# Kernel optimization log

Hardware: AMD Instinct MI355X
Metric: run time of the kernel (lower is better)

## Reference

```python
import jax, jax.numpy as jnp
import numpy as np

D_MODEL = 768
N_HEAD = 12
D_FF = 3072
EPS = 1e-5


def _layer_norm(x, w, b):
    mu = jnp.mean(x, axis=-1, keepdims=True)
    var = jnp.mean(jnp.square(x - mu), axis=-1, keepdims=True)
    return (x - mu) * jax.lax.rsqrt(var + EPS) * w + b


def setup_inputs() -> dict:
    key = jax.random.key(0)
    ks = jax.random.split(key, 8)
    B, S, D = 2, 4096, D_MODEL
    s_in = 1.0 / np.sqrt(D)
    s_ff = 1.0 / np.sqrt(D_FF)
    return {
        "src": jax.random.normal(ks[0], (B, S, D), jnp.float32),
        "w_qkv": jax.random.uniform(ks[1], (3 * D, D), jnp.float32, -s_in, s_in),
        "b_qkv": jnp.zeros((3 * D,), jnp.float32),
        "w_out": jax.random.uniform(ks[2], (D, D), jnp.float32, -s_in, s_in),
        "b_out": jnp.zeros((D,), jnp.float32),
        "w1": jax.random.uniform(ks[3], (D_FF, D), jnp.float32, -s_in, s_in),
        "b1": jnp.zeros((D_FF,), jnp.float32),
        "w2": jax.random.uniform(ks[4], (D, D_FF), jnp.float32, -s_ff, s_ff),
        "b2": jnp.zeros((D,), jnp.float32),
        "ln1_w": jnp.ones((D,), jnp.float32),
        "ln1_b": jnp.zeros((D,), jnp.float32),
        "ln2_w": jnp.ones((D,), jnp.float32),
        "ln2_b": jnp.zeros((D,), jnp.float32),
    }


def reference(src, w_qkv, b_qkv, w_out, b_out, w1, b1, w2, b2,
              ln1_w, ln1_b, ln2_w, ln2_b):
    B, S, D = src.shape
    H, dh = N_HEAD, D // N_HEAD
    # fused QKV projection: [B,S,3D]
    qkv = jnp.einsum('bsd,ed->bse', src, w_qkv) + b_qkv
    q, k, v = jnp.split(qkv, 3, axis=-1)
    q = q.reshape(B, S, H, dh)
    k = k.reshape(B, S, H, dh)
    v = v.reshape(B, S, H, dh)
    scale = 1.0 / np.sqrt(dh)
    scores = jnp.einsum('bqhd,bkhd->bhqk', q, k) * scale  # [B,H,S,S]
    attn = jax.nn.softmax(scores, axis=-1)
    ctx = jnp.einsum('bhqk,bkhd->bqhd', attn, v).reshape(B, S, D)
    attn_out = jnp.einsum('bsd,ed->bse', ctx, w_out) + b_out
    # post-norm residual (norm_first=False), dropout inactive in eval
    x = _layer_norm(src + attn_out, ln1_w, ln1_b)
    h = jax.nn.relu(jnp.einsum('bsd,fd->bsf', x, w1) + b1)
    ffn = jnp.einsum('bsf,df->bsd', h, w2) + b2
    return _layer_norm(x + ffn, ln2_w, ln2_b)
```

## Files before the change

kernel.cpp:

```cpp
#include <hip/hip_runtime.h>
#include <hip/hip_bf16.h>

typedef __hip_bfloat16 bf16;
typedef __attribute__((ext_vector_type(8))) short s16x8;
typedef __attribute__((ext_vector_type(4))) float f32x4;

#define MFMA16x16x32(A, B, C) __builtin_amdgcn_mfma_f32_16x16x32_bf16((A), (B), (C), 0, 0, 0)

__device__ __forceinline__ void async_copy16(const bf16* g, bf16* l) {
  __builtin_amdgcn_global_load_lds(
      (const __attribute__((address_space(1))) void*)g,
      (__attribute__((address_space(3))) void*)l, 16, 0, 0);
}

__device__ __forceinline__ float swz_x16(float x) {
  return __int_as_float(__builtin_amdgcn_ds_swizzle(__float_as_int(x), 0x401f));
}

__device__ __forceinline__ int SW(int row, int chunk) {
  return row * 64 + (((chunk) ^ (row & 7)) << 3);
}

__global__ __launch_bounds__(256)
void cast_f2b_kernel(const float* __restrict__ in, bf16* __restrict__ out, int n) {
  const int i = (blockIdx.x * 256 + threadIdx.x) * 4;
  if (i < n) {
    const float4 f = *(const float4*)(in + i);
    out[i + 0] = (bf16)f.x; out[i + 1] = (bf16)f.y;
    out[i + 2] = (bf16)f.z; out[i + 3] = (bf16)f.w;
  }
}

template <int RELU, int VT, int ACCUM, typename OutT>
__global__ __launch_bounds__(256)
void gemm_bt_kernel(const bf16* __restrict__ A, const bf16* __restrict__ B,
                    const float* __restrict__ bias, OutT* __restrict__ C,
                    int N, int K, int ldb) {
  __shared__ __align__(16) bf16 As[128 * 32];
  __shared__ __align__(16) bf16 Bs[128 * 32];

  const int t = threadIdx.x;
  const int lane = t & 63;
  const int wave = t >> 6;
  const int wm = (wave >> 1) << 6;
  const int wn = (wave & 1) << 6;
  const int col16 = lane & 15;
  const int quad = lane >> 4;
  const int bm = blockIdx.x;
  const int bn = blockIdx.y;

  const bf16* Ag = A + (size_t)(bm * 128 + (t >> 2)) * K + (t & 3) * 8;
  const bf16* Bg = B + (size_t)(bn * 128 + (t >> 2)) * ldb + (t & 3) * 8;
  bf16* Asd = As + t * 8;
  bf16* Bsd = Bs + t * 8;

  f32x4 acc[4][4] = {};

  for (int k0 = 0; k0 < K; k0 += 32) {
    __syncthreads();
    async_copy16(Ag + k0, Asd);
    async_copy16(Ag + (size_t)64 * K + k0, Asd + 2048);
    async_copy16(Bg + k0, Bsd);
    async_copy16(Bg + (size_t)64 * ldb + k0, Bsd + 2048);
    asm volatile("s_waitcnt vmcnt(0)" ::: "memory");
    __syncthreads();

    s16x8 af[4], bfr[4];
#pragma unroll
    for (int i = 0; i < 4; i++)
      af[i] = *(const s16x8*)(As + (wm + i * 16 + col16) * 32 + quad * 8);
#pragma unroll
    for (int j = 0; j < 4; j++)
      bfr[j] = *(const s16x8*)(Bs + (wn + j * 16 + col16) * 32 + quad * 8);
#pragma unroll
    for (int i = 0; i < 4; i++)
#pragma unroll
      for (int j = 0; j < 4; j++)
        acc[i][j] = MFMA16x16x32(af[i], bfr[j], acc[i][j]);
  }

  const int row0 = bm * 128 + wm + quad * 4;
  const int col0 = bn * 128 + wn + col16;
#pragma unroll
  for (int j = 0; j < 4; j++) {
    const int col = col0 + j * 16;
    const float bv = ACCUM ? 0.0f : bias[col];
#pragma unroll
    for (int i = 0; i < 4; i++) {
#pragma unroll
      for (int r = 0; r < 4; r++) {
        float v = acc[i][j][r] + bv;
        if (RELU) v = fmaxf(v, 0.0f);
        const int row = row0 + i * 16 + r;
        if (VT) {
          ((bf16*)C)[(size_t)((row >> 12) * 12 + (col >> 6)) * 262144 +
                     (col & 63) * 4096 + (row & 4095)] = (bf16)v;
        } else {
          const size_t idx = (size_t)row * N + col;
          if (ACCUM) v += ((const float*)C)[idx];
          C[idx] = (OutT)v;
        }
      }
    }
  }
}

__global__ __launch_bounds__(256)
void attn_kernel(const bf16* __restrict__ QK, const bf16* __restrict__ Vt,
                 bf16* __restrict__ ctx) {
  __shared__ __align__(16) bf16 Ks[64 * 64];
  __shared__ __align__(16) bf16 Vs[64 * 64];
  __shared__ __align__(16) bf16 Ps[4][32 * 64];

  const int t = threadIdx.x, lane = t & 63, wave = t >> 6;
  const int col16 = lane & 15, quad = lane >> 4;
  const int b = blockIdx.z, h = blockIdx.y;
  const int qw0 = blockIdx.x * 128 + wave * 32;

  s16x8 bq[2][2];
#pragma unroll
  for (int qt = 0; qt < 2; qt++)
#pragma unroll
    for (int s = 0; s < 2; s++) {
      union { s16x8 v; bf16 hh[8]; } u;
      u.v = *(const s16x8*)(QK + (size_t)(b * 4096 + qw0 + qt * 16 + col16) * 1536 +
                            h * 64 + s * 32 + quad * 8);
#pragma unroll
      for (int e = 0; e < 8; e++) u.hh[e] = (bf16)((float)u.hh[e] * 0.18033688f);
      bq[qt][s] = u.v;
    }

  const bf16* kbase = QK + (size_t)(b * 4096) * 1536 + 768 + h * 64;
  const bf16* vbase = Vt + (size_t)(b * 12 + h) * 262144;
  const int srow = t >> 2;
  const int cch = t & 3;

  f32x4 o[4][2] = {};
  float l_[2] = {0.0f, 0.0f};
  bf16* pw = &Ps[wave][0];

  for (int k0 = 0; k0 < 4096; k0 += 64) {
    const s16x8 kc0 = *(const s16x8*)(kbase + (size_t)(k0 + srow) * 1536 + cch * 8);
    const s16x8 kc1 = *(const s16x8*)(kbase + (size_t)(k0 + srow) * 1536 + cch * 8 + 32);
    const s16x8 vc0 = *(const s16x8*)(vbase + (size_t)srow * 4096 + k0 + cch * 8);
    const s16x8 vc1 = *(const s16x8*)(vbase + (size_t)srow * 4096 + k0 + cch * 8 + 32);
    __syncthreads();
    *(s16x8*)(Ks + SW(srow, cch)) = kc0;
    *(s16x8*)(Ks + SW(srow, cch + 4)) = kc1;
    *(s16x8*)(Vs + SW(srow, cch)) = vc0;
    *(s16x8*)(Vs + SW(srow, cch + 4)) = vc1;
    __syncthreads();

    f32x4 st[4][2] = {};
#pragma unroll
    for (int s = 0; s < 2; s++) {
      s16x8 ak[4];
#pragma unroll
      for (int kt = 0; kt < 4; kt++)
        ak[kt] = *(const s16x8*)(Ks + SW(kt * 16 + col16, s * 4 + quad));
#pragma unroll
      for (int kt = 0; kt < 4; kt++)
#pragma unroll
        for (int qt = 0; qt < 2; qt++)
          st[kt][qt] = MFMA16x16x32(ak[kt], bq[qt][s], st[kt][qt]);
    }

#pragma unroll
    for (int qt = 0; qt < 2; qt++) {
#pragma unroll
      for (int kt = 0; kt < 4; kt++) {
        union { unsigned long long u; bf16 hh[4]; } pk;
#pragma unroll
        for (int r = 0; r < 4; r++) {
          const float p = exp2f(st[kt][qt][r] - 16.0f);
          l_[qt] += p;
          pk.hh[r] = (bf16)p;
        }
        *(unsigned long long*)(pw + (qt * 16 + col16) * 64 +
                               (((kt * 2 + (quad >> 1)) ^ (col16 & 7)) << 3) +
                               (quad & 1) * 4) = pk.u;
      }
    }
    asm volatile("s_waitcnt lgkmcnt(0)" ::: "memory");

#pragma unroll
    for (int s = 0; s < 2; s++) {
      s16x8 bp[2];
#pragma unroll
      for (int qt = 0; qt < 2; qt++)
        bp[qt] = *(const s16x8*)(pw + SW(qt * 16 + col16, s * 4 + quad));
#pragma unroll
      for (int dt = 0; dt < 4; dt++) {
        const s16x8 av = *(const s16x8*)(Vs + SW(dt * 16 + col16, s * 4 + quad));
#pragma unroll
        for (int qt = 0; qt < 2; qt++)
          o[dt][qt] = MFMA16x16x32(av, bp[qt], o[dt][qt]);
      }
    }
  }

  float inv[2];
#pragma unroll
  for (int qt = 0; qt < 2; qt++) {
    float l = l_[qt];
    l += swz_x16(l);
    l += __shfl_xor(l, 32, 64);
    inv[qt] = 1.0f / l;
  }

#pragma unroll
  for (int qt = 0; qt < 2; qt++)
#pragma unroll
    for (int dt = 0; dt < 4; dt++)
#pragma unroll
      for (int r = 0; r < 4; r++)
        pw[(qt * 16 + col16) * 64 + (((dt * 2 + (quad >> 1)) ^ (col16 & 7)) << 3) +
           (quad & 1) * 4 + r] = (bf16)(o[dt][qt][r] * inv[qt]);
  asm volatile("s_waitcnt lgkmcnt(0)" ::: "memory");
  const int qrow = lane >> 1, chalf = (lane & 1) * 4;
  bf16* dst = ctx + (size_t)(b * 4096 + qw0 + qrow) * 768 + h * 64 + chalf * 8;
#pragma unroll
  for (int i = 0; i < 4; i++)
    *(s16x8*)(dst + i * 8) = *(const s16x8*)(pw + SW(qrow, chalf + i));
}

__global__ __launch_bounds__(256)
void add_ln_b_kernel(const float* __restrict__ X, const float* __restrict__ Y,
                     const float* __restrict__ w, const float* __restrict__ b,
                     bf16* __restrict__ out) {
  const int row = blockIdx.x * 4 + (threadIdx.x >> 6);
  const int lane = threadIdx.x & 63;
  const float* x = X + (size_t)row * 768;
  const float* y = Y + (size_t)row * 768;
  float v[12];
  float s = 0.0f;
#pragma unroll
  for (int i = 0; i < 3; i++) {
    const int c = lane * 4 + i * 256;
    const float4 xf = *(const float4*)(x + c);
    const float4 yf = *(const float4*)(y + c);
    v[i * 4 + 0] = xf.x + yf.x; v[i * 4 + 1] = xf.y + yf.y;
    v[i * 4 + 2] = xf.z + yf.z; v[i * 4 + 3] = xf.w + yf.w;
    s += v[i * 4] + v[i * 4 + 1] + v[i * 4 + 2] + v[i * 4 + 3];
  }
#pragma unroll
  for (int off = 32; off > 0; off >>= 1) s += __shfl_xor(s, off, 64);
  const float mu = s * (1.0f / 768.0f);
  float var = 0.0f;
#pragma unroll
  for (int i = 0; i < 12; i++) { const float d = v[i] - mu; var += d * d; }
#pragma unroll
  for (int off = 32; off > 0; off >>= 1) var += __shfl_xor(var, off, 64);
  const float rs = rsqrtf(var * (1.0f / 768.0f) + 1e-5f);
#pragma unroll
  for (int i = 0; i < 12; i++) {
    const int c = lane * 4 + (i >> 2) * 256 + (i & 3);
    out[(size_t)row * 768 + c] = (bf16)((v[i] - mu) * rs * w[c] + b[c]);
  }
}

__global__ __launch_bounds__(256)
void add_ln_f_kernel(const bf16* __restrict__ X, const float* __restrict__ Y,
                     const float* __restrict__ w, const float* __restrict__ b,
                     float* __restrict__ out) {
  const int row = blockIdx.x * 4 + (threadIdx.x >> 6);
  const int lane = threadIdx.x & 63;
  const bf16* x = X + (size_t)row * 768;
  const float* y = Y + (size_t)row * 768;
  float v[12];
  float s = 0.0f;
#pragma unroll
  for (int i = 0; i < 3; i++) {
    const int c = lane * 4 + i * 256;
    const float4 yf = *(const float4*)(y + c);
    v[i * 4 + 0] = (float)x[c + 0] + yf.x; v[i * 4 + 1] = (float)x[c + 1] + yf.y;
    v[i * 4 + 2] = (float)x[c + 2] + yf.z; v[i * 4 + 3] = (float)x[c + 3] + yf.w;
    s += v[i * 4] + v[i * 4 + 1] + v[i * 4 + 2] + v[i * 4 + 3];
  }
#pragma unroll
  for (int off = 32; off > 0; off >>= 1) s += __shfl_xor(s, off, 64);
  const float mu = s * (1.0f / 768.0f);
  float var = 0.0f;
#pragma unroll
  for (int i = 0; i < 12; i++) { const float d = v[i] - mu; var += d * d; }
#pragma unroll
  for (int off = 32; off > 0; off >>= 1) var += __shfl_xor(var, off, 64);
  const float rs = rsqrtf(var * (1.0f / 768.0f) + 1e-5f);
#pragma unroll
  for (int i = 0; i < 12; i++) {
    const int c = lane * 4 + (i >> 2) * 256 + (i & 3);
    out[(size_t)row * 768 + c] = (v[i] - mu) * rs * w[c] + b[c];
  }
}

extern "C" void kernel_launch(void* const* d_in, const int* in_sizes, int n_in,
                              void* d_out, int out_size, void* d_ws, size_t ws_size,
                              hipStream_t stream) {
  (void)in_sizes; (void)n_in; (void)out_size; (void)ws_size;
  const float* src   = (const float*)d_in[0];
  const float* w_qkv = (const float*)d_in[1];
  const float* b_qkv = (const float*)d_in[2];
  const float* w_out = (const float*)d_in[3];
  const float* b_out = (const float*)d_in[4];
  const float* w1    = (const float*)d_in[5];
  const float* b1    = (const float*)d_in[6];
  const float* w2    = (const float*)d_in[7];
  const float* b2    = (const float*)d_in[8];
  const float* ln1w  = (const float*)d_in[9];
  const float* ln1b  = (const float*)d_in[10];
  const float* ln2w  = (const float*)d_in[11];
  const float* ln2b  = (const float*)d_in[12];
  float* out = (float*)d_out;

  char* ws = (char*)d_ws;
  bf16* wqkvb = (bf16*)ws;
  bf16* woutb = (bf16*)(ws + 3538944);
  bf16* w1b   = (bf16*)(ws + 4718592);
  bf16* w2b   = (bf16*)(ws + 9437184);
  bf16* srcb  = (bf16*)(ws + 14155776);
  bf16* QK    = (bf16*)(ws + 26738688);
  bf16* Vt    = (bf16*)(ws + 51904512);
  bf16* ctx   = (bf16*)d_out;
  float* attn_out = (float*)(ws + 26738688);
  bf16* x1b   = (bf16*)(ws + 51904512);
  bf16* hbuf  = (bf16*)(ws + 14155776);
  float* ffn  = out;

  cast_f2b_kernel<<<1728, 256, 0, stream>>>(w_qkv, wqkvb, 2304 * 768);
  cast_f2b_kernel<<<576,  256, 0, stream>>>(w_out, woutb, 768 * 768);
  cast_f2b_kernel<<<2304, 256, 0, stream>>>(w1, w1b, 3072 * 768);
  cast_f2b_kernel<<<2304, 256, 0, stream>>>(w2, w2b, 768 * 3072);
  cast_f2b_kernel<<<6144, 256, 0, stream>>>(src, srcb, 8192 * 768);

  gemm_bt_kernel<0, 0, 0, bf16><<<dim3(64, 12), 256, 0, stream>>>(
      srcb, wqkvb, b_qkv, QK, 1536, 768, 768);
  gemm_bt_kernel<0, 1, 0, bf16><<<dim3(64, 6), 256, 0, stream>>>(
      srcb, wqkvb + (size_t)1536 * 768, b_qkv + 1536, Vt, 768, 768, 768);
  attn_kernel<<<dim3(32, 12, 2), 256, 0, stream>>>(QK, Vt, ctx);
  gemm_bt_kernel<0, 0, 0, float><<<dim3(64, 6), 256, 0, stream>>>(
      ctx, woutb, b_out, attn_out, 768, 768, 768);
  add_ln_b_kernel<<<2048, 256, 0, stream>>>(src, attn_out, ln1w, ln1b, x1b);
  for (int c = 0; c < 2; c++) {
    gemm_bt_kernel<1, 0, 0, bf16><<<dim3(64, 12), 256, 0, stream>>>(
        x1b, w1b + (size_t)c * 1536 * 768, b1 + c * 1536, hbuf, 1536, 768, 768);
    if (c == 0)
      gemm_bt_kernel<0, 0, 0, float><<<dim3(64, 6), 256, 0, stream>>>(
          hbuf, w2b + c * 1536, b2, ffn, 768, 1536, 3072);
    else
      gemm_bt_kernel<0, 0, 1, float><<<dim3(64, 6), 256, 0, stream>>>(
          hbuf, w2b + c * 1536, b2, ffn, 768, 1536, 3072);
  }
  add_ln_f_kernel<<<2048, 256, 0, stream>>>(x1b, ffn, ln2w, ln2b, out);
}
```

Measured before the change: 536.1 us.

## Split attention keys across wave pairs, fuse QKV GEMMs and weight casts

The attention kernel now gives each wave 64 queries and half of each 64-key tile, so K and V fragments loaded from LDS are reused across four query tiles instead of two. The two key-half partial outputs and row sums are merged through LDS at the end, with the partial output rounded to bf16 before the merge. The Q/K and V projection GEMMs are fused into one launch that routes output columns to row-major QK or transposed V, and the five cast launches are merged into one. This cuts LDS traffic and launch count, at the cost of more registers per wave, a slower epilogue where half the waves idle, and some extra rounding error.

```diff
diff --git a/kernel.cpp b/kernel.cpp
--- a/kernel.cpp
+++ b/kernel.cpp
@@ -20,34 +20,40 @@
 __device__ __forceinline__ int SW(int row, int chunk) {
   return row * 64 + (((chunk) ^ (row & 7)) << 3);
 }
-
-__global__ __launch_bounds__(256)
-void cast_f2b_kernel(const float* __restrict__ in, bf16* __restrict__ out, int n) {
-  const int i = (blockIdx.x * 256 + threadIdx.x) * 4;
-  if (i < n) {
-    const float4 f = *(const float4*)(in + i);
-    out[i + 0] = (bf16)f.x; out[i + 1] = (bf16)f.y;
-    out[i + 2] = (bf16)f.z; out[i + 3] = (bf16)f.w;
-  }
-}
-
-template <int RELU, int VT, int ACCUM, typename OutT>
+__device__ __forceinline__ int SW32(int row, int chunk) {
+  return row * 32 + (((chunk) ^ (row & 3)) << 3);
+}
+
+__global__ __launch_bounds__(256)
+void cast_all_kernel(const float* __restrict__ p0, bf16* __restrict__ q0,
+                     const float* __restrict__ p1, bf16* __restrict__ q1,
+                     const float* __restrict__ p2, bf16* __restrict__ q2,
+                     const float* __restrict__ p3, bf16* __restrict__ q3,
+                     const float* __restrict__ p4, bf16* __restrict__ q4) {
+  int blk = blockIdx.x;
+  const float* in; bf16* out;
+  if (blk < 1728)      { in = p0; out = q0; }
+  else if (blk < 2304) { in = p1; out = q1; blk -= 1728; }
+  else if (blk < 4608) { in = p2; out = q2; blk -= 2304; }
+  else if (blk < 6912) { in = p3; out = q3; blk -= 4608; }
+  else                 { in = p4; out = q4; blk -= 6912; }
+  const int i = (blk * 256 + threadIdx.x) * 4;
+  const float4 f = *(const float4*)(in + i);
+  out[i + 0] = (bf16)f.x; out[i + 1] = (bf16)f.y;
+  out[i + 2] = (bf16)f.z; out[i + 3] = (bf16)f.w;
+}
+
+template <int RELU, int ACCUM, typename OutT>
 __global__ __launch_bounds__(256)
 void gemm_bt_kernel(const bf16* __restrict__ A, const bf16* __restrict__ B,
                     const float* __restrict__ bias, OutT* __restrict__ C,
                     int N, int K, int ldb) {
   __shared__ __align__(16) bf16 As[128 * 32];
   __shared__ __align__(16) bf16 Bs[128 * 32];
-
-  const int t = threadIdx.x;
-  const int lane = t & 63;
-  const int wave = t >> 6;
-  const int wm = (wave >> 1) << 6;
-  const int wn = (wave & 1) << 6;
-  const int col16 = lane & 15;
-  const int quad = lane >> 4;
-  const int bm = blockIdx.x;
-  const int bn = blockIdx.y;
+  const int t = threadIdx.x, lane = t & 63, wave = t >> 6;
+  const int wm = (wave >> 1) << 6, wn = (wave & 1) << 6;
+  const int col16 = lane & 15, quad = lane >> 4;
+  const int bm = blockIdx.x, bn = blockIdx.y;
 
   const bf16* Ag = A + (size_t)(bm * 128 + (t >> 2)) * K + (t & 3) * 8;
   const bf16* Bg = B + (size_t)(bn * 128 + (t >> 2)) * ldb + (t & 3) * 8;
@@ -55,7 +61,6 @@
   bf16* Bsd = Bs + t * 8;
 
   f32x4 acc[4][4] = {};
-
   for (int k0 = 0; k0 < K; k0 += 32) {
     __syncthreads();
     async_copy16(Ag + k0, Asd);
@@ -64,7 +69,6 @@
     async_copy16(Bg + (size_t)64 * ldb + k0, Bsd + 2048);
     asm volatile("s_waitcnt vmcnt(0)" ::: "memory");
     __syncthreads();
-
     s16x8 af[4], bfr[4];
 #pragma unroll
     for (int i = 0; i < 4; i++)
@@ -78,7 +82,6 @@
       for (int j = 0; j < 4; j++)
         acc[i][j] = MFMA16x16x32(af[i], bfr[j], acc[i][j]);
   }
-
   const int row0 = bm * 128 + wm + quad * 4;
   const int col0 = bn * 128 + wn + col16;
 #pragma unroll
@@ -86,44 +89,101 @@
     const int col = col0 + j * 16;
     const float bv = ACCUM ? 0.0f : bias[col];
 #pragma unroll
-    for (int i = 0; i < 4; i++) {
+    for (int i = 0; i < 4; i++)
 #pragma unroll
       for (int r = 0; r < 4; r++) {
         float v = acc[i][j][r] + bv;
         if (RELU) v = fmaxf(v, 0.0f);
+        const size_t idx = (size_t)(row0 + i * 16 + r) * N + col;
+        if (ACCUM) v += ((const float*)C)[idx];
+        C[idx] = (OutT)v;
+      }
+  }
+}
+
+__global__ __launch_bounds__(256)
+void gemm_qkv_kernel(const bf16* __restrict__ A, const bf16* __restrict__ B,
+                     const float* __restrict__ bias, bf16* __restrict__ QKo,
+                     bf16* __restrict__ Vt) {
+  __shared__ __align__(16) bf16 As[128 * 32];
+  __shared__ __align__(16) bf16 Bs[128 * 32];
+  const int t = threadIdx.x, lane = t & 63, wave = t >> 6;
+  const int wm = (wave >> 1) << 6, wn = (wave & 1) << 6;
+  const int col16 = lane & 15, quad = lane >> 4;
+  const int bm = blockIdx.x, bn = blockIdx.y;
+  const int K = 768;
+
+  const bf16* Ag = A + (size_t)(bm * 128 + (t >> 2)) * K + (t & 3) * 8;
+  const bf16* Bg = B + (size_t)(bn * 128 + (t >> 2)) * K + (t & 3) * 8;
+  bf16* Asd = As + t * 8;
+  bf16* Bsd = Bs + t * 8;
+
+  f32x4 acc[4][4] = {};
+  for (int k0 = 0; k0 < K; k0 += 32) {
+    __syncthreads();
+    async_copy16(Ag + k0, Asd);
+    async_copy16(Ag + (size_t)64 * K + k0, Asd + 2048);
+    async_copy16(Bg + k0, Bsd);
+    async_copy16(Bg + (size_t)64 * K + k0, Bsd + 2048);
+    asm volatile("s_waitcnt vmcnt(0)" ::: "memory");
+    __syncthreads();
+    s16x8 af[4], bfr[4];
+#pragma unroll
+    for (int i = 0; i < 4; i++)
+      af[i] = *(const s16x8*)(As + (wm + i * 16 + col16) * 32 + quad * 8);
+#pragma unroll
+    for (int j = 0; j < 4; j++)
+      bfr[j] = *(const s16x8*)(Bs + (wn + j * 16 + col16) * 32 + quad * 8);
+#pragma unroll
+    for (int i = 0; i < 4; i++)
+#pragma unroll
+      for (int j = 0; j < 4; j++)
+        acc[i][j] = MFMA16x16x32(af[i], bfr[j], acc[i][j]);
+  }
+  const int row0 = bm * 128 + wm + quad * 4;
+  const int col0 = bn * 128 + wn + col16;
+#pragma unroll
+  for (int j = 0; j < 4; j++) {
+    const int col = col0 + j * 16;
+    const float bv = bias[col];
+#pragma unroll
+    for (int i = 0; i < 4; i++)
+#pragma unroll
+      for (int r = 0; r < 4; r++) {
+        const float v = acc[i][j][r] + bv;
         const int row = row0 + i * 16 + r;
-        if (VT) {
-          ((bf16*)C)[(size_t)((row >> 12) * 12 + (col >> 6)) * 262144 +
-                     (col & 63) * 4096 + (row & 4095)] = (bf16)v;
+        if (bn < 12) {
+          QKo[(size_t)row * 1536 + col] = (bf16)v;
         } else {
-          const size_t idx = (size_t)row * N + col;
-          if (ACCUM) v += ((const float*)C)[idx];
-          C[idx] = (OutT)v;
+          const int vc = col - 1536;
+          Vt[(size_t)((row >> 12) * 12 + (vc >> 6)) * 262144 +
+             (vc & 63) * 4096 + (row & 4095)] = (bf16)v;
         }
       }
-    }
   }
 }
 
 __global__ __launch_bounds__(256)
 void attn_kernel(const bf16* __restrict__ QK, const bf16* __restrict__ Vt,
                  bf16* __restrict__ ctx) {
-  __shared__ __align__(16) bf16 Ks[64 * 64];
-  __shared__ __align__(16) bf16 Vs[64 * 64];
-  __shared__ __align__(16) bf16 Ps[4][32 * 64];
+  __shared__ __align__(16) bf16 lds[16384];
+  bf16* Ks = lds;
+  bf16* Vs = lds + 4096;
+  bf16* Ps = lds + 8192;
 
   const int t = threadIdx.x, lane = t & 63, wave = t >> 6;
   const int col16 = lane & 15, quad = lane >> 4;
+  const int qh = wave >> 1, kh = wave & 1;
   const int b = blockIdx.z, h = blockIdx.y;
-  const int qw0 = blockIdx.x * 128 + wave * 32;
-
-  s16x8 bq[2][2];
-#pragma unroll
-  for (int qt = 0; qt < 2; qt++)
+  const int qbase = blockIdx.x * 128 + qh * 64;
+
+  s16x8 bq[4][2];
+#pragma unroll
+  for (int qt = 0; qt < 4; qt++)
 #pragma unroll
     for (int s = 0; s < 2; s++) {
       union { s16x8 v; bf16 hh[8]; } u;
-      u.v = *(const s16x8*)(QK + (size_t)(b * 4096 + qw0 + qt * 16 + col16) * 1536 +
+      u.v = *(const s16x8*)(QK + (size_t)(b * 4096 + qbase + qt * 16 + col16) * 1536 +
                             h * 64 + s * 32 + quad * 8);
 #pragma unroll
       for (int e = 0; e < 8; e++) u.hh[e] = (bf16)((float)u.hh[e] * 0.18033688f);
@@ -132,12 +192,11 @@
 
   const bf16* kbase = QK + (size_t)(b * 4096) * 1536 + 768 + h * 64;
   const bf16* vbase = Vt + (size_t)(b * 12 + h) * 262144;
-  const int srow = t >> 2;
-  const int cch = t & 3;
-
-  f32x4 o[4][2] = {};
-  float l_[2] = {0.0f, 0.0f};
-  bf16* pw = &Ps[wave][0];
+  const int srow = t >> 2, cch = t & 3;
+
+  f32x4 o[4][4] = {};
+  float l_[4] = {};
+  bf16* pw = Ps + wave * 2048;
 
   for (int k0 = 0; k0 < 4096; k0 += 64) {
     const s16x8 kc0 = *(const s16x8*)(kbase + (size_t)(k0 + srow) * 1536 + cch * 8);
@@ -151,24 +210,25 @@
     *(s16x8*)(Vs + SW(srow, cch + 4)) = vc1;
     __syncthreads();
 
-    f32x4 st[4][2] = {};
+    f32x4 st[2][4] = {};
 #pragma unroll
     for (int s = 0; s < 2; s++) {
-      s16x8 ak[4];
-#pragma unroll
-      for (int kt = 0; kt < 4; kt++)
-        ak[kt] = *(const s16x8*)(Ks + SW(kt * 16 + col16, s * 4 + quad));
-#pragma unroll
-      for (int kt = 0; kt < 4; kt++)
-#pragma unroll
-        for (int qt = 0; qt < 2; qt++)
+      s16x8 ak[2];
+#pragma unroll
+      for (int kt = 0; kt < 2; kt++)
+        ak[kt] = *(const s16x8*)(Ks + SW(kh * 32 + kt * 16 + col16, s * 4 + quad));
+#pragma unroll
+      for (int kt = 0; kt < 2; kt++)
+#pragma unroll
+        for (int qt = 0; qt < 4; qt++)
           st[kt][qt] = MFMA16x16x32(ak[kt], bq[qt][s], st[kt][qt]);
     }
 
 #pragma unroll
-    for (int qt = 0; qt < 2; qt++) {
-#pragma unroll
-      for (int kt = 0; kt < 4; kt++) {
+    for (int qt = 0; qt < 4; qt++) {
+      const int q32 = qt * 16 + col16;
+#pragma unroll
+      for (int kt = 0; kt < 2; kt++) {
         union { unsigned long long u; bf16 hh[4]; } pk;
 #pragma unroll
         for (int r = 0; r < 4; r++) {
@@ -176,52 +236,84 @@
           l_[qt] += p;
           pk.hh[r] = (bf16)p;
         }
-        *(unsigned long long*)(pw + (qt * 16 + col16) * 64 +
-                               (((kt * 2 + (quad >> 1)) ^ (col16 & 7)) << 3) +
+        const int chunk = kt * 2 + (quad >> 1);
+        *(unsigned long long*)(pw + q32 * 32 + ((chunk ^ (q32 & 3)) << 3) +
                                (quad & 1) * 4) = pk.u;
       }
     }
     asm volatile("s_waitcnt lgkmcnt(0)" ::: "memory");
 
-#pragma unroll
-    for (int s = 0; s < 2; s++) {
-      s16x8 bp[2];
-#pragma unroll
-      for (int qt = 0; qt < 2; qt++)
-        bp[qt] = *(const s16x8*)(pw + SW(qt * 16 + col16, s * 4 + quad));
+    s16x8 bp[4];
+#pragma unroll
+    for (int qt = 0; qt < 4; qt++)
+      bp[qt] = *(const s16x8*)(pw + SW32(qt * 16 + col16, quad));
+#pragma unroll
+    for (int dt = 0; dt < 4; dt++) {
+      const s16x8 av = *(const s16x8*)(Vs + SW(dt * 16 + col16, kh * 4 + quad));
+#pragma unroll
+      for (int qt = 0; qt < 4; qt++)
+        o[dt][qt] = MFMA16x16x32(av, bp[qt], o[dt][qt]);
+    }
+  }
+
+  __syncthreads();
+  bf16* mb = lds;
+  float* lb = (float*)(lds + 8192);
+  if (kh == 1) {
+#pragma unroll
+    for (int qt = 0; qt < 4; qt++) {
+      const int q = qt * 16 + col16;
+#pragma unroll
+      for (int dt = 0; dt < 4; dt++)
+#pragma unroll
+        for (int r = 0; r < 4; r++)
+          mb[qh * 4096 + q * 64 + dt * 16 + quad * 4 + r] = (bf16)o[dt][qt][r];
+      lb[qh * 1024 + q * 4 + quad] = l_[qt];
+    }
+  }
+  __syncthreads();
+  if (kh == 0) {
+    float inv[4];
+#pragma unroll
+    for (int qt = 0; qt < 4; qt++) {
+      const int q = qt * 16 + col16;
+      float l = l_[qt] + lb[qh * 1024 + q * 4 + quad];
+      l += swz_x16(l);
+      l += __shfl_xor(l, 32, 64);
+      inv[qt] = 1.0f / l;
+    }
+#pragma unroll
+    for (int qt = 0; qt < 4; qt++) {
+      const int q = qt * 16 + col16;
+#pragma unroll
+      for (int dt = 0; dt < 4; dt++)
+#pragma unroll
+        for (int r = 0; r < 4; r++)
+          o[dt][qt][r] += (float)mb[qh * 4096 + q * 64 + dt * 16 + quad * 4 + r];
+    }
+    asm volatile("s_waitcnt lgkmcnt(0)" ::: "memory");
+    bf16* tr = lds + 8192 + qh * 4096;
+#pragma unroll
+    for (int qt = 0; qt < 4; qt++) {
+      const int q = qt * 16 + col16;
 #pragma unroll
       for (int dt = 0; dt < 4; dt++) {
-        const s16x8 av = *(const s16x8*)(Vs + SW(dt * 16 + col16, s * 4 + quad));
-#pragma unroll
-        for (int qt = 0; qt < 2; qt++)
-          o[dt][qt] = MFMA16x16x32(av, bp[qt], o[dt][qt]);
+        union { unsigned long long u; bf16 hh[4]; } pk;
+#pragma unroll
+        for (int r = 0; r < 4; r++) pk.hh[r] = (bf16)(o[dt][qt][r] * inv[qt]);
+        const int chunk = dt * 2 + (quad >> 1);
+        *(unsigned long long*)(tr + q * 64 + ((chunk ^ (q & 7)) << 3) +
+                               (quad & 1) * 4) = pk.u;
       }
     }
-  }
-
-  float inv[2];
-#pragma unroll
-  for (int qt = 0; qt < 2; qt++) {
-    float l = l_[qt];
-    l += swz_x16(l);
-    l += __shfl_xor(l, 32, 64);
-    inv[qt] = 1.0f / l;
-  }
-
-#pragma unroll
-  for (int qt = 0; qt < 2; qt++)
-#pragma unroll
-    for (int dt = 0; dt < 4; dt++)
-#pragma unroll
-      for (int r = 0; r < 4; r++)
-        pw[(qt * 16 + col16) * 64 + (((dt * 2 + (quad >> 1)) ^ (col16 & 7)) << 3) +
-           (quad & 1) * 4 + r] = (bf16)(o[dt][qt][r] * inv[qt]);
-  asm volatile("s_waitcnt lgkmcnt(0)" ::: "memory");
-  const int qrow = lane >> 1, chalf = (lane & 1) * 4;
-  bf16* dst = ctx + (size_t)(b * 4096 + qw0 + qrow) * 768 + h * 64 + chalf * 8;
-#pragma unroll
-  for (int i = 0; i < 4; i++)
-    *(s16x8*)(dst + i * 8) = *(const s16x8*)(pw + SW(qrow, chalf + i));
+    asm volatile("s_waitcnt lgkmcnt(0)" ::: "memory");
+    bf16* dst = ctx + (size_t)(b * 4096 + qbase + lane) * 768 + h * 64;
+#pragma unroll
+    for (int p = 0; p < 8; p++) {
+      const s16x8 val = *(const s16x8*)(tr + lane * 64 + (p << 3));
+      *(s16x8*)(dst + (p ^ (lane & 7)) * 8) = val;
+    }
+  }
 }
 
 __global__ __launch_bounds__(256)
@@ -232,16 +324,14 @@
   const int lane = threadIdx.x & 63;
   const float* x = X + (size_t)row * 768;
   const float* y = Y + (size_t)row * 768;
-  float v[12];
-  float s = 0.0f;
+  float v[12]; float s = 0.0f;
 #pragma unroll
   for (int i = 0; i < 3; i++) {
     const int c = lane * 4 + i * 256;
     const float4 xf = *(const float4*)(x + c);
     const float4 yf = *(const float4*)(y + c);
-    v[i * 4 + 0] = xf.x + yf.x; v[i * 4 + 1] = xf.y + yf.y;
-    v[i * 4 + 2] = xf.z + yf.z; v[i * 4 + 3] = xf.w + yf.w;
-    s += v[i * 4] + v[i * 4 + 1] + v[i * 4 + 2] + v[i * 4 + 3];
+    v[i*4+0]=xf.x+yf.x; v[i*4+1]=xf.y+yf.y; v[i*4+2]=xf.z+yf.z; v[i*4+3]=xf.w+yf.w;
+    s += v[i*4]+v[i*4+1]+v[i*4+2]+v[i*4+3];
   }
 #pragma unroll
   for (int off = 32; off > 0; off >>= 1) s += __shfl_xor(s, off, 64);
@@ -267,15 +357,14 @@
   const int lane = threadIdx.x & 63;
   const bf16* x = X + (size_t)row * 768;
   const float* y = Y + (size_t)row * 768;
-  float v[12];
-  float s = 0.0f;
+  float v[12]; float s = 0.0f;
 #pragma unroll
   for (int i = 0; i < 3; i++) {
     const int c = lane * 4 + i * 256;
     const float4 yf = *(const float4*)(y + c);
-    v[i * 4 + 0] = (float)x[c + 0] + yf.x; v[i * 4 + 1] = (float)x[c + 1] + yf.y;
-    v[i * 4 + 2] = (float)x[c + 2] + yf.z; v[i * 4 + 3] = (float)x[c + 3] + yf.w;
-    s += v[i * 4] + v[i * 4 + 1] + v[i * 4 + 2] + v[i * 4 + 3];
+    v[i*4+0]=(float)x[c+0]+yf.x; v[i*4+1]=(float)x[c+1]+yf.y;
+    v[i*4+2]=(float)x[c+2]+yf.z; v[i*4+3]=(float)x[c+3]+yf.w;
+    s += v[i*4]+v[i*4+1]+v[i*4+2]+v[i*4+3];
   }
 #pragma unroll
   for (int off = 32; off > 0; off >>= 1) s += __shfl_xor(s, off, 64);
@@ -326,28 +415,21 @@
   bf16* hbuf  = (bf16*)(ws + 14155776);
   float* ffn  = out;
 
-  cast_f2b_kernel<<<1728, 256, 0, stream>>>(w_qkv, wqkvb, 2304 * 768);
-  cast_f2b_kernel<<<576,  256, 0, stream>>>(w_out, woutb, 768 * 768);
-  cast_f2b_kernel<<<2304, 256, 0, stream>>>(w1, w1b, 3072 * 768);
-  cast_f2b_kernel<<<2304, 256, 0, stream>>>(w2, w2b, 768 * 3072);
-  cast_f2b_kernel<<<6144, 256, 0, stream>>>(src, srcb, 8192 * 768);
-
-  gemm_bt_kernel<0, 0, 0, bf16><<<dim3(64, 12), 256, 0, stream>>>(
-      srcb, wqkvb, b_qkv, QK, 1536, 768, 768);
-  gemm_bt_kernel<0, 1, 0, bf16><<<dim3(64, 6), 256, 0, stream>>>(
-      srcb, wqkvb + (size_t)1536 * 768, b_qkv + 1536, Vt, 768, 768, 768);
+  cast_all_kernel<<<13056, 256, 0, stream>>>(w_qkv, wqkvb, w_out, woutb,
+                                             w1, w1b, w2, w2b, src, srcb);
+  gemm_qkv_kernel<<<dim3(64, 18), 256, 0, stream>>>(srcb, wqkvb, b_qkv, QK, Vt);
   attn_kernel<<<dim3(32, 12, 2), 256, 0, stream>>>(QK, Vt, ctx);
-  gemm_bt_kernel<0, 0, 0, float><<<dim3(64, 6), 256, 0, stream>>>(
+  gemm_bt_kernel<0, 0, float><<<dim3(64, 6), 256, 0, stream>>>(
       ctx, woutb, b_out, attn_out, 768, 768, 768);
   add_ln_b_kernel<<<2048, 256, 0, stream>>>(src, attn_out, ln1w, ln1b, x1b);
   for (int c = 0; c < 2; c++) {
-    gemm_bt_kernel<1, 0, 0, bf16><<<dim3(64, 12), 256, 0, stream>>>(
+    gemm_bt_kernel<1, 0, bf16><<<dim3(64, 12), 256, 0, stream>>>(
         x1b, w1b + (size_t)c * 1536 * 768, b1 + c * 1536, hbuf, 1536, 768, 768);
     if (c == 0)
-      gemm_bt_kernel<0, 0, 0, float><<<dim3(64, 6), 256, 0, stream>>>(
+      gemm_bt_kernel<0, 0, float><<<dim3(64, 6), 256, 0, stream>>>(
           hbuf, w2b + c * 1536, b2, ffn, 768, 1536, 3072);
     else
-      gemm_bt_kernel<0, 0, 1, float><<<dim3(64, 6), 256, 0, stream>>>(
+      gemm_bt_kernel<0, 1, float><<<dim3(64, 6), 256, 0, stream>>>(
           hbuf, w2b + c * 1536, b2, ffn, 768, 1536, 3072);
   }
   add_ln_f_kernel<<<2048, 256, 0, stream>>>(x1b, ffn, ln2w, ln2b, out);
```

Measured after the change: 608.4 us. +13.5%, slower.
